# Optimization experiments

Measured on AMD Instinct MI355X. Metric: run time of the kernel, lower is better.

The kernel has to match this reference:

```python
import jax, jax.numpy as jnp
import numpy as np

B, N, D = 1, 2048, 2048
H, DH, DR, MP = 16, 128, 64, 4
LOCAL = H * DH // MP  # per-shard qkv width
ATTN_MASK_VALUE = -1e10
LN_EPS = 1e-5


def setup_inputs() -> dict:
    key = jax.random.key(0)
    ks = jax.random.split(key, 5)
    s = 0.02
    return {
        "x": jax.random.normal(ks[0], (B, N, D), jnp.float32),
        "ln_scale": jnp.ones((D,), jnp.float32),
        "ln_offset": jnp.zeros((D,), jnp.float32),
        "w_qkv": jax.random.normal(ks[1], (D, 3 * H * DH), jnp.float32) * s,
        "w_attn_out": jax.random.normal(ks[2], (H * DH, D), jnp.float32) * s,
        "w_ff_in": jax.random.normal(ks[3], (D, 4 * D), jnp.float32) * s,
        "b_ff_in": jnp.zeros((4 * D,), jnp.float32),
        "w_ff_out": jax.random.normal(ks[4], (4 * D, D), jnp.float32) * s,
        "b_ff_out": jnp.zeros((D,), jnp.float32),
    }


def _rotate_every_two(x):
    # (..., d) -> interleaved (-x2, x1) pairs, GPT-J style
    x1 = x[..., ::2]
    x2 = x[..., 1::2]
    return jnp.stack((-x2, x1), axis=-1).reshape(x.shape)


def _fixed_pos_embedding(n, dim):
    inv_freq = 1.0 / (10000.0 ** (np.arange(0, dim, 2, dtype=np.float32) / dim))
    ang = np.einsum("i,j->ij", np.arange(n, dtype=np.float32), inv_freq)  # [n, dim/2]
    return jnp.asarray(np.sin(ang), jnp.float32), jnp.asarray(np.cos(ang), jnp.float32)


def _apply_rotary(x, sin, cos):
    # x: [b, n, h, d_rot]; sin/cos: [n, d_rot/2] repeated pairwise -> [1, n, 1, d_rot]
    sin = jnp.repeat(sin, 2, axis=-1)[None, :, None, :]
    cos = jnp.repeat(cos, 2, axis=-1)[None, :, None, :]
    return x * cos + _rotate_every_two(x) * sin


def reference(x, ln_scale, ln_offset, w_qkv, w_attn_out, w_ff_in, b_ff_in, w_ff_out, b_ff_out):
    # ---- LayerNorm (shared input to parallel attn + FFN) ----
    mu = jnp.mean(x, axis=-1, keepdims=True)
    var = jnp.var(x, axis=-1, keepdims=True)
    h = (x - mu) * jax.lax.rsqrt(var + LN_EPS) * ln_scale + ln_offset

    # ---- Causal self-attention with partial rotary ----
    qkv = (h @ w_qkv).reshape(B, N, MP, 3 * LOCAL)  # mp-sharded layout
    q, v, k = jnp.split(qkv, [LOCAL, 2 * LOCAL], axis=-1)
    heads = lambda t: t.reshape(B, N, H, DH)  # shard_heads: [b,n,mp,local] -> [b,n,h,dh]
    q, v, k = heads(q), heads(v), heads(k)

    sin, cos = _fixed_pos_embedding(N, DR)
    q = jnp.concatenate([_apply_rotary(q[..., :DR], sin, cos), q[..., DR:]], axis=-1)
    k = jnp.concatenate([_apply_rotary(k[..., :DR], sin, cos), k[..., DR:]], axis=-1)

    attn_scale = np.float32(np.sqrt(DH))
    logits = jnp.einsum("bihd,bjhd->bhij", q, k) / attn_scale
    causal_mask = jnp.triu(jnp.ones((N, N), dtype=bool), 1)
    logits = jnp.where(causal_mask, ATTN_MASK_VALUE, logits)
    attn_w = jax.nn.softmax(logits, axis=-1)
    attn_vec = jnp.einsum("bhij,bjhd->bihd", attn_w, v).reshape(B, N, H * DH)
    attn_out = attn_vec @ w_attn_out

    # ---- FFN (parallel branch, same LN input) ----
    ff_out = jax.nn.gelu(h @ w_ff_in + b_ff_in) @ w_ff_out + b_ff_out

    return attn_out + ff_out
```

## Files before the change

### kernel.cpp

```cpp
#include <hip/hip_runtime.h>
#include <hip/hip_bf16.h>

using bf16_t = __hip_bfloat16;
typedef __attribute__((ext_vector_type(8))) __bf16 bfrag;
typedef __attribute__((ext_vector_type(4))) float f32x4;

#define MFMA16(a, b, c) __builtin_amdgcn_mfma_f32_16x16x32_bf16((a), (b), (c), 0, 0, 0)

__device__ __forceinline__ void gload_lds16(const void* g, void* l) {
  __builtin_amdgcn_global_load_lds((const __attribute__((address_space(1))) void*)g,
                                   (__attribute__((address_space(3))) void*)l, 16, 0, 0);
}

__global__ __launch_bounds__(256) void transpose_cvt(const float* __restrict__ in,
    bf16_t* __restrict__ out, int K, int N) {
  __shared__ float t[32][33];
  const int n0 = blockIdx.x * 32, k0 = blockIdx.y * 32;
  const int tx = threadIdx.x & 31, ty = threadIdx.x >> 5;
#pragma unroll
  for (int i = 0; i < 4; ++i)
    t[ty + i * 8][tx] = in[(size_t)(k0 + ty + i * 8) * N + n0 + tx];
  __syncthreads();
#pragma unroll
  for (int i = 0; i < 4; ++i)
    out[(size_t)(n0 + ty + i * 8) * K + k0 + tx] = bf16_t(t[tx][ty + i * 8]);
}

__global__ __launch_bounds__(256) void ln_kernel(const float* __restrict__ x,
    const float* __restrict__ sc, const float* __restrict__ of, bf16_t* __restrict__ h) {
  __shared__ float red[8];
  const int n = blockIdx.x, tid = threadIdx.x;
  const float* xr = x + (size_t)n * 2048;
  float4 a = ((const float4*)xr)[tid * 2];
  float4 b = ((const float4*)xr)[tid * 2 + 1];
  float s = a.x + a.y + a.z + a.w + b.x + b.y + b.z + b.w;
  float q = a.x * a.x + a.y * a.y + a.z * a.z + a.w * a.w +
            b.x * b.x + b.y * b.y + b.z * b.z + b.w * b.w;
#pragma unroll
  for (int m = 32; m; m >>= 1) { s += __shfl_xor(s, m); q += __shfl_xor(q, m); }
  if ((tid & 63) == 0) { red[(tid >> 6) * 2] = s; red[(tid >> 6) * 2 + 1] = q; }
  __syncthreads();
  s = red[0] + red[2] + red[4] + red[6];
  q = red[1] + red[3] + red[5] + red[7];
  const float mu = s * (1.f / 2048.f);
  const float inv = rsqrtf(q * (1.f / 2048.f) - mu * mu + 1e-5f);
  const int base = tid * 8;
  float v[8] = {a.x, a.y, a.z, a.w, b.x, b.y, b.z, b.w};
  bf16_t* hr = h + (size_t)n * 2048 + base;
#pragma unroll
  for (int j = 0; j < 8; ++j) hr[j] = bf16_t((v[j] - mu) * inv * sc[base + j] + of[base + j]);
}

template <int EPI>
__global__ __launch_bounds__(512, 2) void gemm8p(
    const bf16_t* __restrict__ A, int lda, const bf16_t* __restrict__ BT, int ldb,
    const float* __restrict__ bias, float* __restrict__ Cf, bf16_t* __restrict__ Cb,
    int M, int N, int K, size_t splitStride) {
  extern __shared__ __align__(16) char lds[];
  const int tid = threadIdx.x, wid = tid >> 6, lane = tid & 63;
  const int lc = lane & 15, lg = lane >> 4;
  const int bm = blockIdx.y * 256, bn = blockIdx.x * 256;
  const int wr = wid >> 2, wc = wid & 3;
  const int NT = K >> 6;
  const int sr = wid * 16 + (lane >> 2);
  const int lgp = (lane & 3) ^ ((sr >> 1) & 3);
  const size_t rA = (size_t)128 * lda, rB = (size_t)128 * ldb;
  const bf16_t* pA0 = A + (size_t)blockIdx.z * K + (size_t)(bm + sr) * lda + lgp * 8;
  const bf16_t* pA1 = pA0 + 32;
  const bf16_t* pB0 = BT + (size_t)blockIdx.z * K + (size_t)(bn + sr) * ldb + lgp * 8;
  const bf16_t* pB1 = pB0 + 32;
  auto stA0 = [&](int ts) { char* b = lds + (((ts & 1) * 2 + 0) << 14) + wid * 1024;
    gload_lds16(pA0, b); gload_lds16(pA0 + rA, b + 8192); pA0 += 64; };
  auto stA1 = [&](int ts) { char* b = lds + (((ts & 1) * 2 + 1) << 14) + wid * 1024;
    gload_lds16(pA1, b); gload_lds16(pA1 + rA, b + 8192); pA1 += 64; };
  auto stB0 = [&](int ts) { char* b = lds + 65536 + (((ts & 1) * 2 + 0) << 14) + wid * 1024;
    gload_lds16(pB0, b); gload_lds16(pB0 + rB, b + 8192); pB0 += 64; };
  auto stB1 = [&](int ts) { char* b = lds + 65536 + (((ts & 1) * 2 + 1) << 14) + wid * 1024;
    gload_lds16(pB1, b); gload_lds16(pB1 + rB, b + 8192); pB1 += 64; };

  stA0(0); stB0(0); stA1(0); stB1(0); stA0(1); stB0(1); stA1(1);
  asm volatile("s_waitcnt vmcnt(6)" ::: "memory");
  __builtin_amdgcn_s_barrier();

  f32x4 acc[8][4] = {};
#define FR(off, row) \
  (*(const bfrag*)(lds + (off) + (row) * 64 + ((lg ^ (((row) >> 1) & 3)) << 4)))

  for (int t = 0; t < NT; ++t) {
    const int d = t & 1;
    const int aoff0 = (d * 2 + 0) << 14, aoff1 = (d * 2 + 1) << 14;
    const int boff0 = 65536 + aoff0, boff1 = 65536 + aoff1;
    bfrag a[8];
    {
#pragma unroll
      for (int m = 0; m < 8; ++m) a[m] = FR(aoff0, wr * 128 + m * 16 + lc);
      bfrag b0 = FR(boff0, wc * 64 + lc);
      bfrag b1 = FR(boff0, wc * 64 + 16 + lc);
      if (t + 1 < NT) stB1(t + 1);
      __builtin_amdgcn_s_barrier();
      asm volatile("s_waitcnt lgkmcnt(0)" ::: "memory");
      __builtin_amdgcn_sched_barrier(0);
      __builtin_amdgcn_s_setprio(1);
#pragma unroll
      for (int m = 0; m < 8; ++m) {
        acc[m][0] = MFMA16(a[m], b0, acc[m][0]);
        acc[m][1] = MFMA16(a[m], b1, acc[m][1]);
      }
      __builtin_amdgcn_s_setprio(0);
      __builtin_amdgcn_s_barrier();
    }
    {
      bfrag b2 = FR(boff0, wc * 64 + 32 + lc);
      bfrag b3 = FR(boff0, wc * 64 + 48 + lc);
      if (t + 2 < NT) stA0(t + 2);
      __builtin_amdgcn_s_barrier();
      asm volatile("s_waitcnt lgkmcnt(0)" ::: "memory");
      __builtin_amdgcn_sched_barrier(0);
      __builtin_amdgcn_s_setprio(1);
#pragma unroll
      for (int m = 0; m < 8; ++m) {
        acc[m][2] = MFMA16(a[m], b2, acc[m][2]);
        acc[m][3] = MFMA16(a[m], b3, acc[m][3]);
      }
      __builtin_amdgcn_s_setprio(0);
      __builtin_amdgcn_s_barrier();
    }
    {
#pragma unroll
      for (int m = 0; m < 8; ++m) a[m] = FR(aoff1, wr * 128 + m * 16 + lc);
      bfrag b0 = FR(boff1, wc * 64 + lc);
      bfrag b1 = FR(boff1, wc * 64 + 16 + lc);
      if (t + 2 < NT) stB0(t + 2);
      __builtin_amdgcn_s_barrier();
      asm volatile("s_waitcnt lgkmcnt(0)" ::: "memory");
      __builtin_amdgcn_sched_barrier(0);
      __builtin_amdgcn_s_setprio(1);
#pragma unroll
      for (int m = 0; m < 8; ++m) {
        acc[m][0] = MFMA16(a[m], b0, acc[m][0]);
        acc[m][1] = MFMA16(a[m], b1, acc[m][1]);
      }
      __builtin_amdgcn_s_setprio(0);
      __builtin_amdgcn_s_barrier();
    }
    {
      bfrag b2 = FR(boff1, wc * 64 + 32 + lc);
      bfrag b3 = FR(boff1, wc * 64 + 48 + lc);
      if (t + 2 < NT) stA1(t + 2);
      __builtin_amdgcn_s_barrier();
      asm volatile("s_waitcnt lgkmcnt(0)" ::: "memory");
      __builtin_amdgcn_sched_barrier(0);
      __builtin_amdgcn_s_setprio(1);
#pragma unroll
      for (int m = 0; m < 8; ++m) {
        acc[m][2] = MFMA16(a[m], b2, acc[m][2]);
        acc[m][3] = MFMA16(a[m], b3, acc[m][3]);
      }
      __builtin_amdgcn_s_setprio(0);
      if (t < NT - 2) asm volatile("s_waitcnt vmcnt(6)" ::: "memory");
      else            asm volatile("s_waitcnt vmcnt(0)" ::: "memory");
      __builtin_amdgcn_s_barrier();
    }
  }
#undef FR
  char* W = lds + wid * 16384;
  if (EPI & 8) {
    bf16_t* Wb = (bf16_t*)W;
#pragma unroll
    for (int mc = 0; mc < 2; ++mc) {
#pragma unroll
      for (int m4 = 0; m4 < 4; ++m4) {
#pragma unroll
        for (int n = 0; n < 4; ++n) {
          const int col = bn + wc * 64 + n * 16 + lc;
          float bv = (EPI & 1) ? bias[col] : 0.f;
#pragma unroll
          for (int i = 0; i < 4; ++i) {
            float v = acc[mc * 4 + m4][n][i];
            if (EPI & 1) v += bv;
            if (EPI & 2) v = 0.5f * v * (1.f + tanhf(0.7978845608028654f * (v + 0.044715f * v * v * v)));
            Wb[(m4 * 16 + lg * 4 + i) * 72 + n * 16 + lc] = bf16_t(v);
          }
        }
      }
      asm volatile("s_waitcnt lgkmcnt(0)" ::: "memory");
      __builtin_amdgcn_sched_barrier(0);
#pragma unroll
      for (int p = 0; p < 8; ++p) {
        const int rl = p * 8 + (lane >> 3), j = lane & 7;
        uint4 v = *(const uint4*)&Wb[rl * 72 + j * 8];
        const int grow = bm + wr * 128 + mc * 64 + rl;
        const int gcol = bn + wc * 64 + j * 8;
        *(uint4*)&Cb[(size_t)grow * N + gcol] = v;
      }
      asm volatile("s_waitcnt lgkmcnt(0)" ::: "memory");
      __builtin_amdgcn_sched_barrier(0);
    }
  } else {
    float* Wf = (float*)W;
    float* Cfz = Cf + (size_t)blockIdx.z * splitStride;
#pragma unroll
    for (int mc = 0; mc < 4; ++mc) {
#pragma unroll
      for (int m2 = 0; m2 < 2; ++m2) {
#pragma unroll
        for (int n = 0; n < 4; ++n) {
          const int col = bn + wc * 64 + n * 16 + lc;
          float bv = (EPI & 1) ? bias[col] : 0.f;
#pragma unroll
          for (int i = 0; i < 4; ++i) {
            float v = acc[mc * 2 + m2][n][i];
            if (EPI & 1) v += bv;
            if (EPI & 2) v = 0.5f * v * (1.f + tanhf(0.7978845608028654f * (v + 0.044715f * v * v * v)));
            Wf[(m2 * 16 + lg * 4 + i) * 72 + n * 16 + lc] = v;
          }
        }
      }
      asm volatile("s_waitcnt lgkmcnt(0)" ::: "memory");
      __builtin_amdgcn_sched_barrier(0);
#pragma unroll
      for (int p = 0; p < 8; ++p) {
        const int rl = p * 4 + (lane >> 4), j = lane & 15;
        float4 v = *(const float4*)&Wf[rl * 72 + j * 4];
        const int grow = bm + wr * 128 + mc * 32 + rl;
        const int gcol = bn + wc * 64 + j * 4;
        *(float4*)&Cfz[(size_t)grow * N + gcol] = v;
      }
      asm volatile("s_waitcnt lgkmcnt(0)" ::: "memory");
      __builtin_amdgcn_sched_barrier(0);
    }
  }
}

template <int NP, bool ADDIN, bool BIAS>
__global__ __launch_bounds__(256) void reduceP(const float* __restrict__ p0,
    const float* __restrict__ p1, const float* __restrict__ p2,
    const float* __restrict__ p3, const float* __restrict__ bias,
    float* __restrict__ out, int total, int colmask) {
  const int i = (blockIdx.x * 256 + threadIdx.x) * 4;
  if (i >= total) return;
  float4 v = *(const float4*)(p0 + i);
  float4 w = *(const float4*)(p1 + i);
  v.x += w.x; v.y += w.y; v.z += w.z; v.w += w.w;
  if (NP == 4) {
    float4 u = *(const float4*)(p2 + i);
    float4 z = *(const float4*)(p3 + i);
    v.x += u.x + z.x; v.y += u.y + z.y; v.z += u.z + z.z; v.w += u.w + z.w;
  }
  if (BIAS) {
    float4 b = *(const float4*)(bias + (i & colmask));
    v.x += b.x; v.y += b.y; v.z += b.z; v.w += b.w;
  }
  if (ADDIN) {
    float4 o = *(const float4*)(out + i);
    v.x += o.x; v.y += o.y; v.z += o.z; v.w += o.w;
  }
  *(float4*)(out + i) = v;
}

__global__ __launch_bounds__(128) void rope_kernel(const bf16_t* __restrict__ qkv,
    bf16_t* __restrict__ qh, bf16_t* __restrict__ kh, bf16_t* __restrict__ vT) {
  const int n = blockIdx.x, hh = blockIdx.y;
  const int d = threadIdx.x;
  const int mp = hh >> 2, hi = hh & 3;
  const bf16_t* row = qkv + (size_t)n * 6144 + mp * 1536 + hi * 128;
  float q = __bfloat162float(row[d]);
  float k = __bfloat162float(row[1024 + d]);
  if (d < 64) {
    const float ang = (float)n * powf(10000.f, -(float)(d & ~1) / 64.f);
    const float sn = sinf(ang), cs = cosf(ang);
    const float qp = __shfl_xor(q, 1), kp = __shfl_xor(k, 1);
    if (d & 1) { q = q * cs + qp * sn; k = k * cs + kp * sn; }
    else       { q = q * cs - qp * sn; k = k * cs - kp * sn; }
  }
  qh[((size_t)hh * 2048 + n) * 128 + d] = bf16_t(q * 0.08838834764831845f);
  kh[((size_t)hh * 2048 + n) * 128 + d] = bf16_t(k);
  vT[((size_t)hh * 128 + d) * 2048 + n] = row[512 + d];
}

__global__ __launch_bounds__(256) void attn_kernel(const bf16_t* __restrict__ qh,
    const bf16_t* __restrict__ kh, const bf16_t* __restrict__ vT,
    bf16_t* __restrict__ Op, float2* __restrict__ ml) {
  __shared__ alignas(16) char Kbuf[2][16384];
  __shared__ alignas(16) char Vbuf[2][16384];
  __shared__ alignas(16) bf16_t Ps[4][16 * 72];
  const int p = blockIdx.x, h = blockIdx.y, z = blockIdx.z;
  const int tid = threadIdx.x, wid = tid >> 6, lane = tid & 63;
  const int lc = lane & 15, lg = lane >> 4;
  const int krow = wid * 4 + (lane >> 4);
  const int vrow = wid * 8 + (lane >> 3);

  auto stage = [&](int kv0, int d) {
#pragma unroll
    for (int i = 0; i < 4; ++i) {
      const int kr = i * 16 + krow;
      const int kch = (lane & 15) ^ (kr & 15);
      gload_lds16(kh + ((size_t)h * 2048 + kv0 + kr) * 128 + kch * 8,
                  Kbuf[d] + i * 4096 + wid * 1024);
      const int vr = i * 32 + vrow;
      const int vch = (lane & 7) ^ (vr & 7);
      gload_lds16(vT + ((size_t)h * 128 + vr) * 2048 + kv0 + vch * 8,
                  Vbuf[d] + i * 4096 + wid * 1024);
    }
  };
#define FRK(d, row, ch) (*(const bfrag*)(Kbuf[d] + (row) * 256 + (((ch) ^ ((row) & 15)) << 4)))
#define FRV(d, row, ch) (*(const bfrag*)(Vbuf[d] + (row) * 128 + (((ch) ^ ((row) & 7)) << 4)))

#pragma unroll 1
  for (int half = 0; half < 2; ++half) {
    const int qt = half ? (31 - p) : p;
    const int nkv = qt + 1;
    const int lo = (z * nkv) / 3, hi = ((z + 1) * nkv) / 3;
    const int nj = hi - lo;
    const int qr = qt * 64 + wid * 16;
    const bf16_t* Qb = qh + ((size_t)h * 2048 + qr) * 128;
    bfrag qf[4];
#pragma unroll
    for (int ks = 0; ks < 4; ++ks)
      qf[ks] = *(const bfrag*)&Qb[lc * 128 + ks * 32 + lg * 8];
    f32x4 O[8] = {};
    float mr[4] = {-1e30f, -1e30f, -1e30f, -1e30f};
    float lsum[4] = {0.f, 0.f, 0.f, 0.f};

    if (nj > 0) {
      stage(lo * 64, 0);
      asm volatile("s_waitcnt vmcnt(0)" ::: "memory");
      __builtin_amdgcn_s_barrier();
    }
#pragma unroll 1
    for (int j = 0; j < nj; ++j) {
      const int kt = lo + j, d = j & 1;
      const int kv0 = kt * 64;
      if (j + 1 < nj) stage(kv0 + 64, d ^ 1);
      f32x4 s[4];
#pragma unroll
      for (int c = 0; c < 4; ++c) {
        f32x4 a = {};
#pragma unroll
        for (int ks = 0; ks < 4; ++ks) {
          bfrag kf = FRK(d, c * 16 + lc, ks * 4 + lg);
          a = MFMA16(qf[ks], kf, a);
        }
        s[c] = a;
      }
      if (kt == qt) {
#pragma unroll
        for (int c = 0; c < 4; ++c)
#pragma unroll
          for (int i = 0; i < 4; ++i)
            if (kv0 + c * 16 + lc > qr + lg * 4 + i) s[c][i] = -1e10f;
      }
      float pm[4];
#pragma unroll
      for (int i = 0; i < 4; ++i)
        pm[i] = fmaxf(fmaxf(s[0][i], s[1][i]), fmaxf(s[2][i], s[3][i]));
#pragma unroll
      for (int m = 1; m < 16; m <<= 1)
#pragma unroll
        for (int i = 0; i < 4; ++i) pm[i] = fmaxf(pm[i], __shfl_xor(pm[i], m));
      float al[4], rs[4];
#pragma unroll
      for (int i = 0; i < 4; ++i) {
        const float mn = fmaxf(mr[i], pm[i]);
        al[i] = __expf(mr[i] - mn);
        mr[i] = mn;
        rs[i] = 0.f;
      }
#pragma unroll
      for (int c = 0; c < 4; ++c)
#pragma unroll
        for (int i = 0; i < 4; ++i) {
          const float pv = __expf(s[c][i] - mr[i]);
          s[c][i] = pv; rs[i] += pv;
        }
#pragma unroll
      for (int m = 1; m < 16; m <<= 1)
#pragma unroll
        for (int i = 0; i < 4; ++i) rs[i] += __shfl_xor(rs[i], m);
#pragma unroll
      for (int i = 0; i < 4; ++i) lsum[i] = lsum[i] * al[i] + rs[i];
#pragma unroll
      for (int n = 0; n < 8; ++n)
#pragma unroll
        for (int i = 0; i < 4; ++i) O[n][i] *= al[i];
#pragma unroll
      for (int c = 0; c < 4; ++c)
#pragma unroll
        for (int i = 0; i < 4; ++i)
          Ps[wid][(lg * 4 + i) * 72 + c * 16 + lc] = bf16_t(s[c][i]);
#pragma unroll
      for (int k2 = 0; k2 < 2; ++k2) {
        bfrag pf = *(const bfrag*)((const char*)&Ps[wid][0] + lc * 144 + k2 * 64 + lg * 16);
#pragma unroll
        for (int n = 0; n < 8; ++n) {
          bfrag vf = FRV(d, n * 16 + lc, k2 * 4 + lg);
          O[n] = MFMA16(pf, vf, O[n]);
        }
      }
      if (j + 1 < nj) asm volatile("s_waitcnt vmcnt(0)" ::: "memory");
      asm volatile("s_waitcnt lgkmcnt(0)" ::: "memory");
      __builtin_amdgcn_s_barrier();
    }
    const size_t rb = (size_t)(z * 16 + h) * 2048 + qr;
#pragma unroll
    for (int n = 0; n < 8; ++n)
#pragma unroll
      for (int i = 0; i < 4; ++i)
        Op[(rb + lg * 4 + i) * 128 + n * 16 + lc] = bf16_t(O[n][i]);
    if (lc == 0) {
#pragma unroll
      for (int i = 0; i < 4; ++i)
        ml[rb + lg * 4 + i] = make_float2(mr[i], lsum[i]);
    }
    __builtin_amdgcn_s_barrier();
  }
#undef FRK
#undef FRV
}

__global__ __launch_bounds__(256) void attn_combine(const bf16_t* __restrict__ Op,
    const float2* __restrict__ ml, bf16_t* __restrict__ av) {
  const int idx = blockIdx.x * 256 + threadIdx.x;
  const int t = idx & 15, hr = idx >> 4;
  const int ZS = 16 * 2048;
  const size_t ZO = (size_t)ZS * 128;
  const float2 m0 = ml[hr], m1 = ml[ZS + hr], m2 = ml[2 * ZS + hr];
  const float M = fmaxf(fmaxf(m0.x, m1.x), m2.x);
  const float w0 = __expf(m0.x - M), w1 = __expf(m1.x - M), w2 = __expf(m2.x - M);
  const float inv = 1.f / (w0 * m0.y + w1 * m1.y + w2 * m2.y);
  const bf16_t* p0 = Op + (size_t)hr * 128 + t * 8;
  uint4 a0 = *(const uint4*)p0;
  uint4 a1 = *(const uint4*)(p0 + ZO);
  uint4 a2 = *(const uint4*)(p0 + 2 * ZO);
  const unsigned* u0 = (const unsigned*)&a0;
  const unsigned* u1 = (const unsigned*)&a1;
  const unsigned* u2 = (const unsigned*)&a2;
  bf16_t ov[8];
#pragma unroll
  for (int j = 0; j < 8; ++j) {
    const int w = j >> 1, sh = (j & 1) * 16;
    const float f0 = __uint_as_float(((u0[w] >> sh) & 0xffffu) << 16);
    const float f1 = __uint_as_float(((u1[w] >> sh) & 0xffffu) << 16);
    const float f2 = __uint_as_float(((u2[w] >> sh) & 0xffffu) << 16);
    ov[j] = bf16_t((w0 * f0 + w1 * f1 + w2 * f2) * inv);
  }
  const int row = hr & 2047, hh = hr >> 11;
  *(uint4*)(av + (size_t)row * 2048 + hh * 128 + t * 8) = *(const uint4*)ov;
}

extern "C" void kernel_launch(void* const* d_in, const int* in_sizes, int n_in,
                              void* d_out, int out_size, void* d_ws, size_t ws_size,
                              hipStream_t stream) {
  const float* x        = (const float*)d_in[0];
  const float* ln_scale = (const float*)d_in[1];
  const float* ln_offset= (const float*)d_in[2];
  const float* w_qkv    = (const float*)d_in[3];
  const float* w_ao     = (const float*)d_in[4];
  const float* w_ff_in  = (const float*)d_in[5];
  const float* b_ff_in  = (const float*)d_in[6];
  const float* w_ff_out = (const float*)d_in[7];
  const float* b_ff_out = (const float*)d_in[8];
  float* out = (float*)d_out;

  char* ws = (char*)d_ws;
  bf16_t* wqkvT   = (bf16_t*)(ws);
  bf16_t* waoT    = (bf16_t*)(ws + 25165824);
  bf16_t* wffinT  = (bf16_t*)(ws + 33554432);
  bf16_t* wffoutT = (bf16_t*)(ws + 67108864);
  bf16_t* h       = (bf16_t*)(ws + 100663296);
  bf16_t* qhb     = (bf16_t*)(ws + 109051904);
  bf16_t* khb     = (bf16_t*)(ws + 117440512);
  bf16_t* vTb     = (bf16_t*)(ws + 125829120);
  bf16_t* avb     = (bf16_t*)(ws + 134217728);
  bf16_t* qkvb    = (bf16_t*)(ws + 142606336);
  bf16_t* ff1b    = qkvb;
  float*  pa      = (float*)(ws + 142606336);
  float*  pf      = (float*)(ws);
  bf16_t* Opart   = (bf16_t*)(ws);
  float2* mlpart  = (float2*)(ws + 142606336 + 25165824);

  hipFuncSetAttribute((const void*)gemm8p<0>,  hipFuncAttributeMaxDynamicSharedMemorySize, 131072);
  hipFuncSetAttribute((const void*)gemm8p<8>,  hipFuncAttributeMaxDynamicSharedMemorySize, 131072);
  hipFuncSetAttribute((const void*)gemm8p<11>, hipFuncAttributeMaxDynamicSharedMemorySize, 131072);

  dim3 b256(256), b512(512);
  transpose_cvt<<<dim3(192, 64),  b256, 0, stream>>>(w_qkv,    wqkvT,   2048, 6144);
  transpose_cvt<<<dim3(64, 64),   b256, 0, stream>>>(w_ao,     waoT,    2048, 2048);
  transpose_cvt<<<dim3(256, 64),  b256, 0, stream>>>(w_ff_in,  wffinT,  2048, 8192);
  transpose_cvt<<<dim3(64, 256),  b256, 0, stream>>>(w_ff_out, wffoutT, 8192, 2048);
  ln_kernel<<<dim3(2048), b256, 0, stream>>>(x, ln_scale, ln_offset, h);

  gemm8p<8><<<dim3(24, 8, 1), b512, 131072, stream>>>(h, 2048, wqkvT, 2048,
      nullptr, nullptr, qkvb, 2048, 6144, 2048, 0);
  rope_kernel<<<dim3(2048, 16), dim3(128), 0, stream>>>(qkvb, qhb, khb, vTb);

  attn_kernel<<<dim3(16, 16, 3), b256, 0, stream>>>(qhb, khb, vTb, Opart, mlpart);
  attn_combine<<<dim3(2048), b256, 0, stream>>>(Opart, mlpart, avb);

  gemm8p<0><<<dim3(8, 8, 2), b512, 131072, stream>>>(avb, 2048, waoT, 2048,
      nullptr, pa, nullptr, 2048, 2048, 1024, (size_t)2048 * 2048);
  reduceP<2, false, false><<<dim3(4096), b256, 0, stream>>>(pa, pa + 4194304,
      nullptr, nullptr, nullptr, out, 4194304, 2047);

  gemm8p<11><<<dim3(32, 8, 1), b512, 131072, stream>>>(h, 2048, wffinT, 2048,
      b_ff_in, nullptr, ff1b, 2048, 8192, 2048, 0);

  gemm8p<0><<<dim3(8, 8, 4), b512, 131072, stream>>>(ff1b, 8192, wffoutT, 8192,
      nullptr, pf, nullptr, 2048, 2048, 2048, (size_t)2048 * 2048);
  reduceP<4, true, true><<<dim3(4096), b256, 0, stream>>>(pf, pf + 4194304,
      pf + 2 * 4194304, pf + 3 * 4194304, b_ff_out, out, 4194304, 2047);
}
```

Measured before the change: 437.3 us.

## Restructure GEMM pipeline to 2-phase, split attn-out GEMM 4-way with bf16 partials

The GEMM main loop goes from four half-tile phases with staggered loads to two full-tile phases, each issuing a full next-stage A+B load, with fewer barriers and waits per k-tile. The attention output projection becomes a 4-way split-K GEMM that writes bf16 partials, reduced by a new reduce4b kernel, instead of a 2-way fp32 split. The weight transpose kernel now uses 64x64 tiles with float4 loads and 8-byte stores. Together these aim to cut barrier overhead, raise parallelism for the small GEMM and improve transpose bandwidth, at the cost of coarser load/compute overlap and bf16 rounding of the partial sums.

```diff
diff --git a/kernel.cpp b/kernel.cpp
--- a/kernel.cpp
+++ b/kernel.cpp
@@ -12,18 +12,28 @@
                                    (__attribute__((address_space(3))) void*)l, 16, 0, 0);
 }
 
+__device__ __forceinline__ float bf2f(unsigned u) { return __uint_as_float(u << 16); }
+
 __global__ __launch_bounds__(256) void transpose_cvt(const float* __restrict__ in,
     bf16_t* __restrict__ out, int K, int N) {
-  __shared__ float t[32][33];
-  const int n0 = blockIdx.x * 32, k0 = blockIdx.y * 32;
-  const int tx = threadIdx.x & 31, ty = threadIdx.x >> 5;
-#pragma unroll
-  for (int i = 0; i < 4; ++i)
-    t[ty + i * 8][tx] = in[(size_t)(k0 + ty + i * 8) * N + n0 + tx];
+  __shared__ float t[64][65];
+  const int n0 = blockIdx.x * 64, k0 = blockIdx.y * 64;
+  const int tx = threadIdx.x & 15, ty = threadIdx.x >> 4;
+#pragma unroll
+  for (int i = 0; i < 4; ++i) {
+    float4 v = *(const float4*)&in[(size_t)(k0 + i * 16 + ty) * N + n0 + tx * 4];
+    t[i * 16 + ty][tx * 4 + 0] = v.x; t[i * 16 + ty][tx * 4 + 1] = v.y;
+    t[i * 16 + ty][tx * 4 + 2] = v.z; t[i * 16 + ty][tx * 4 + 3] = v.w;
+  }
   __syncthreads();
 #pragma unroll
-  for (int i = 0; i < 4; ++i)
-    out[(size_t)(n0 + ty + i * 8) * K + k0 + tx] = bf16_t(t[tx][ty + i * 8]);
+  for (int i = 0; i < 4; ++i) {
+    const int n = i * 16 + ty;
+    bf16_t w[4];
+#pragma unroll
+    for (int j = 0; j < 4; ++j) w[j] = bf16_t(t[tx * 4 + j][n]);
+    *(uint2*)&out[(size_t)(n0 + n) * K + k0 + tx * 4] = *(const uint2*)w;
+  }
 }
 
 __global__ __launch_bounds__(256) void ln_kernel(const float* __restrict__ x,
@@ -52,7 +62,7 @@
 }
 
 template <int EPI>
-__global__ __launch_bounds__(512, 2) void gemm8p(
+__global__ __launch_bounds__(512, 2) void gemm2p(
     const bf16_t* __restrict__ A, int lda, const bf16_t* __restrict__ BT, int ldb,
     const float* __restrict__ bias, float* __restrict__ Cf, bf16_t* __restrict__ Cb,
     int M, int N, int K, size_t splitStride) {
@@ -78,8 +88,8 @@
   auto stB1 = [&](int ts) { char* b = lds + 65536 + (((ts & 1) * 2 + 1) << 14) + wid * 1024;
     gload_lds16(pB1, b); gload_lds16(pB1 + rB, b + 8192); pB1 += 64; };
 
-  stA0(0); stB0(0); stA1(0); stB1(0); stA0(1); stB0(1); stA1(1);
-  asm volatile("s_waitcnt vmcnt(6)" ::: "memory");
+  stA0(0); stB0(0); stA1(0); stB1(0); stA0(1); stB0(1);
+  asm volatile("s_waitcnt vmcnt(8)" ::: "memory");
   __builtin_amdgcn_s_barrier();
 
   f32x4 acc[8][4] = {};
@@ -90,74 +100,43 @@
     const int d = t & 1;
     const int aoff0 = (d * 2 + 0) << 14, aoff1 = (d * 2 + 1) << 14;
     const int boff0 = 65536 + aoff0, boff1 = 65536 + aoff1;
-    bfrag a[8];
     {
+      bfrag a[8], b[4];
 #pragma unroll
       for (int m = 0; m < 8; ++m) a[m] = FR(aoff0, wr * 128 + m * 16 + lc);
-      bfrag b0 = FR(boff0, wc * 64 + lc);
-      bfrag b1 = FR(boff0, wc * 64 + 16 + lc);
-      if (t + 1 < NT) stB1(t + 1);
+#pragma unroll
+      for (int n = 0; n < 4; ++n) b[n] = FR(boff0, wc * 64 + n * 16 + lc);
+      if (t + 1 < NT) { stA1(t + 1); stB1(t + 1); }
       __builtin_amdgcn_s_barrier();
       asm volatile("s_waitcnt lgkmcnt(0)" ::: "memory");
       __builtin_amdgcn_sched_barrier(0);
       __builtin_amdgcn_s_setprio(1);
 #pragma unroll
-      for (int m = 0; m < 8; ++m) {
-        acc[m][0] = MFMA16(a[m], b0, acc[m][0]);
-        acc[m][1] = MFMA16(a[m], b1, acc[m][1]);
-      }
+      for (int m = 0; m < 8; ++m)
+#pragma unroll
+        for (int n = 0; n < 4; ++n) acc[m][n] = MFMA16(a[m], b[n], acc[m][n]);
       __builtin_amdgcn_s_setprio(0);
+      if (t < NT - 2) asm volatile("s_waitcnt vmcnt(8)" ::: "memory");
+      else            asm volatile("s_waitcnt vmcnt(0)" ::: "memory");
       __builtin_amdgcn_s_barrier();
     }
     {
-      bfrag b2 = FR(boff0, wc * 64 + 32 + lc);
-      bfrag b3 = FR(boff0, wc * 64 + 48 + lc);
-      if (t + 2 < NT) stA0(t + 2);
+      bfrag a[8], b[4];
+#pragma unroll
+      for (int m = 0; m < 8; ++m) a[m] = FR(aoff1, wr * 128 + m * 16 + lc);
+#pragma unroll
+      for (int n = 0; n < 4; ++n) b[n] = FR(boff1, wc * 64 + n * 16 + lc);
+      if (t + 2 < NT) { stA0(t + 2); stB0(t + 2); }
       __builtin_amdgcn_s_barrier();
       asm volatile("s_waitcnt lgkmcnt(0)" ::: "memory");
       __builtin_amdgcn_sched_barrier(0);
       __builtin_amdgcn_s_setprio(1);
 #pragma unroll
-      for (int m = 0; m < 8; ++m) {
-        acc[m][2] = MFMA16(a[m], b2, acc[m][2]);
-        acc[m][3] = MFMA16(a[m], b3, acc[m][3]);
-      }
+      for (int m = 0; m < 8; ++m)
+#pragma unroll
+        for (int n = 0; n < 4; ++n) acc[m][n] = MFMA16(a[m], b[n], acc[m][n]);
       __builtin_amdgcn_s_setprio(0);
-      __builtin_amdgcn_s_barrier();
-    }
-    {
-#pragma unroll
-      for (int m = 0; m < 8; ++m) a[m] = FR(aoff1, wr * 128 + m * 16 + lc);
-      bfrag b0 = FR(boff1, wc * 64 + lc);
-      bfrag b1 = FR(boff1, wc * 64 + 16 + lc);
-      if (t + 2 < NT) stB0(t + 2);
-      __builtin_amdgcn_s_barrier();
-      asm volatile("s_waitcnt lgkmcnt(0)" ::: "memory");
-      __builtin_amdgcn_sched_barrier(0);
-      __builtin_amdgcn_s_setprio(1);
-#pragma unroll
-      for (int m = 0; m < 8; ++m) {
-        acc[m][0] = MFMA16(a[m], b0, acc[m][0]);
-        acc[m][1] = MFMA16(a[m], b1, acc[m][1]);
-      }
-      __builtin_amdgcn_s_setprio(0);
-      __builtin_amdgcn_s_barrier();
-    }
-    {
-      bfrag b2 = FR(boff1, wc * 64 + 32 + lc);
-      bfrag b3 = FR(boff1, wc * 64 + 48 + lc);
-      if (t + 2 < NT) stA1(t + 2);
-      __builtin_amdgcn_s_barrier();
-      asm volatile("s_waitcnt lgkmcnt(0)" ::: "memory");
-      __builtin_amdgcn_sched_barrier(0);
-      __builtin_amdgcn_s_setprio(1);
-#pragma unroll
-      for (int m = 0; m < 8; ++m) {
-        acc[m][2] = MFMA16(a[m], b2, acc[m][2]);
-        acc[m][3] = MFMA16(a[m], b3, acc[m][3]);
-      }
-      __builtin_amdgcn_s_setprio(0);
-      if (t < NT - 2) asm volatile("s_waitcnt vmcnt(6)" ::: "memory");
+      if (t < NT - 2) asm volatile("s_waitcnt vmcnt(8)" ::: "memory");
       else            asm volatile("s_waitcnt vmcnt(0)" ::: "memory");
       __builtin_amdgcn_s_barrier();
     }
@@ -166,6 +145,7 @@
   char* W = lds + wid * 16384;
   if (EPI & 8) {
     bf16_t* Wb = (bf16_t*)W;
+    bf16_t* Cbz = Cb + (size_t)blockIdx.z * splitStride;
 #pragma unroll
     for (int mc = 0; mc < 2; ++mc) {
 #pragma unroll
@@ -191,7 +171,7 @@
         uint4 v = *(const uint4*)&Wb[rl * 72 + j * 8];
         const int grow = bm + wr * 128 + mc * 64 + rl;
         const int gcol = bn + wc * 64 + j * 8;
-        *(uint4*)&Cb[(size_t)grow * N + gcol] = v;
+        *(uint4*)&Cbz[(size_t)grow * N + gcol] = v;
       }
       asm volatile("s_waitcnt lgkmcnt(0)" ::: "memory");
       __builtin_amdgcn_sched_barrier(0);
@@ -256,6 +236,30 @@
     v.x += o.x; v.y += o.y; v.z += o.z; v.w += o.w;
   }
   *(float4*)(out + i) = v;
+}
+
+__global__ __launch_bounds__(256) void reduce4b(const bf16_t* __restrict__ p0,
+    const bf16_t* __restrict__ p1, const bf16_t* __restrict__ p2,
+    const bf16_t* __restrict__ p3, float* __restrict__ out, int total) {
+  const int i = (blockIdx.x * 256 + threadIdx.x) * 8;
+  if (i >= total) return;
+  uint4 a0 = *(const uint4*)(p0 + i);
+  uint4 a1 = *(const uint4*)(p1 + i);
+  uint4 a2 = *(const uint4*)(p2 + i);
+  uint4 a3 = *(const uint4*)(p3 + i);
+  const unsigned* u0 = (const unsigned*)&a0;
+  const unsigned* u1 = (const unsigned*)&a1;
+  const unsigned* u2 = (const unsigned*)&a2;
+  const unsigned* u3 = (const unsigned*)&a3;
+  float r[8];
+#pragma unroll
+  for (int j = 0; j < 8; ++j) {
+    const int w = j >> 1, sh = (j & 1) * 16;
+    r[j] = bf2f((u0[w] >> sh) & 0xffffu) + bf2f((u1[w] >> sh) & 0xffffu) +
+           bf2f((u2[w] >> sh) & 0xffffu) + bf2f((u3[w] >> sh) & 0xffffu);
+  }
+  *(float4*)(out + i) = make_float4(r[0], r[1], r[2], r[3]);
+  *(float4*)(out + i + 4) = make_float4(r[4], r[5], r[6], r[7]);
 }
 
 __global__ __launch_bounds__(128) void rope_kernel(const bf16_t* __restrict__ qkv,
@@ -439,10 +443,9 @@
 #pragma unroll
   for (int j = 0; j < 8; ++j) {
     const int w = j >> 1, sh = (j & 1) * 16;
-    const float f0 = __uint_as_float(((u0[w] >> sh) & 0xffffu) << 16);
-    const float f1 = __uint_as_float(((u1[w] >> sh) & 0xffffu) << 16);
-    const float f2 = __uint_as_float(((u2[w] >> sh) & 0xffffu) << 16);
-    ov[j] = bf16_t((w0 * f0 + w1 * f1 + w2 * f2) * inv);
+    ov[j] = bf16_t((w0 * bf2f((u0[w] >> sh) & 0xffffu) +
+                    w1 * bf2f((u1[w] >> sh) & 0xffffu) +
+                    w2 * bf2f((u2[w] >> sh) & 0xffffu)) * inv);
   }
   const int row = hr & 2047, hh = hr >> 11;
   *(uint4*)(av + (size_t)row * 2048 + hh * 128 + t * 8) = *(const uint4*)ov;
@@ -474,38 +477,38 @@
   bf16_t* avb     = (bf16_t*)(ws + 134217728);
   bf16_t* qkvb    = (bf16_t*)(ws + 142606336);
   bf16_t* ff1b    = qkvb;
-  float*  pa      = (float*)(ws + 142606336);
+  bf16_t* pab     = qkvb;
   float*  pf      = (float*)(ws);
   bf16_t* Opart   = (bf16_t*)(ws);
-  float2* mlpart  = (float2*)(ws + 142606336 + 25165824);
-
-  hipFuncSetAttribute((const void*)gemm8p<0>,  hipFuncAttributeMaxDynamicSharedMemorySize, 131072);
-  hipFuncSetAttribute((const void*)gemm8p<8>,  hipFuncAttributeMaxDynamicSharedMemorySize, 131072);
-  hipFuncSetAttribute((const void*)gemm8p<11>, hipFuncAttributeMaxDynamicSharedMemorySize, 131072);
+  float2* mlpart  = (float2*)(ws + 167772160);
+
+  hipFuncSetAttribute((const void*)gemm2p<0>,  hipFuncAttributeMaxDynamicSharedMemorySize, 131072);
+  hipFuncSetAttribute((const void*)gemm2p<8>,  hipFuncAttributeMaxDynamicSharedMemorySize, 131072);
+  hipFuncSetAttribute((const void*)gemm2p<11>, hipFuncAttributeMaxDynamicSharedMemorySize, 131072);
 
   dim3 b256(256), b512(512);
-  transpose_cvt<<<dim3(192, 64),  b256, 0, stream>>>(w_qkv,    wqkvT,   2048, 6144);
-  transpose_cvt<<<dim3(64, 64),   b256, 0, stream>>>(w_ao,     waoT,    2048, 2048);
-  transpose_cvt<<<dim3(256, 64),  b256, 0, stream>>>(w_ff_in,  wffinT,  2048, 8192);
-  transpose_cvt<<<dim3(64, 256),  b256, 0, stream>>>(w_ff_out, wffoutT, 8192, 2048);
+  transpose_cvt<<<dim3(96, 32),  b256, 0, stream>>>(w_qkv,    wqkvT,   2048, 6144);
+  transpose_cvt<<<dim3(32, 32),  b256, 0, stream>>>(w_ao,     waoT,    2048, 2048);
+  transpose_cvt<<<dim3(128, 32), b256, 0, stream>>>(w_ff_in,  wffinT,  2048, 8192);
+  transpose_cvt<<<dim3(32, 128), b256, 0, stream>>>(w_ff_out, wffoutT, 8192, 2048);
   ln_kernel<<<dim3(2048), b256, 0, stream>>>(x, ln_scale, ln_offset, h);
 
-  gemm8p<8><<<dim3(24, 8, 1), b512, 131072, stream>>>(h, 2048, wqkvT, 2048,
+  gemm2p<8><<<dim3(24, 8, 1), b512, 131072, stream>>>(h, 2048, wqkvT, 2048,
       nullptr, nullptr, qkvb, 2048, 6144, 2048, 0);
   rope_kernel<<<dim3(2048, 16), dim3(128), 0, stream>>>(qkvb, qhb, khb, vTb);
 
   attn_kernel<<<dim3(16, 16, 3), b256, 0, stream>>>(qhb, khb, vTb, Opart, mlpart);
   attn_combine<<<dim3(2048), b256, 0, stream>>>(Opart, mlpart, avb);
 
-  gemm8p<0><<<dim3(8, 8, 2), b512, 131072, stream>>>(avb, 2048, waoT, 2048,
-      nullptr, pa, nullptr, 2048, 2048, 1024, (size_t)2048 * 2048);
-  reduceP<2, false, false><<<dim3(4096), b256, 0, stream>>>(pa, pa + 4194304,
-      nullptr, nullptr, nullptr, out, 4194304, 2047);
-
-  gemm8p<11><<<dim3(32, 8, 1), b512, 131072, stream>>>(h, 2048, wffinT, 2048,
+  gemm2p<8><<<dim3(8, 8, 4), b512, 131072, stream>>>(avb, 2048, waoT, 2048,
+      nullptr, nullptr, pab, 2048, 2048, 512, (size_t)2048 * 2048);
+  reduce4b<<<dim3(2048), b256, 0, stream>>>(pab, pab + 4194304, pab + 2 * 4194304,
+      pab + 3 * 4194304, out, 4194304);
+
+  gemm2p<11><<<dim3(32, 8, 1), b512, 131072, stream>>>(h, 2048, wffinT, 2048,
       b_ff_in, nullptr, ff1b, 2048, 8192, 2048, 0);
 
-  gemm8p<0><<<dim3(8, 8, 4), b512, 131072, stream>>>(ff1b, 8192, wffoutT, 8192,
+  gemm2p<0><<<dim3(8, 8, 4), b512, 131072, stream>>>(ff1b, 8192, wffoutT, 8192,
       nullptr, pf, nullptr, 2048, 2048, 2048, (size_t)2048 * 2048);
   reduceP<4, true, true><<<dim3(4096), b256, 0, stream>>>(pf, pf + 4194304,
       pf + 2 * 4194304, pf + 3 * 4194304, b_ff_out, out, 4194304, 2047);
```

Result: faster. 421.8 us (-3.5%).
